# Performance work log

Hardware: AMD Instinct MI355X
Metric: run time of the kernel (lower is better)

## Reference

```python
import jax, jax.numpy as jnp
import numpy as np

# Hard-coded constants from the original module
GAMMA = 0.1      # self.gamma default
N_STEPS = 10     # self.n_steps default
RHO = 0.9        # RMSProp decay
LR = 0.009       # RMSProp learning rate
MOM = 0.9        # momentum
EPS = 1e-8       # RMSProp epsilon
ABS_EPS = 1e-6   # diff_abs smoothing: diff_abs(x) = sqrt(x^2 + 1e-6)

B, IN_DIM, OUT_DIM = 4096, 2048, 4096


def setup_inputs() -> dict:
    key = jax.random.key(0)
    k1, k2 = jax.random.split(key)
    inputs = jax.random.normal(k1, (B, IN_DIM), dtype=jnp.float32)
    # keras 'uniform' init: U(-0.05, 0.05), shape (output_dim, input_dim)
    W = jax.random.uniform(k2, (OUT_DIM, IN_DIM), minval=-0.05, maxval=0.05, dtype=jnp.float32)
    return {"inputs": inputs, "W": W}


def reference(inputs, W):
    batch = inputs.shape[0]
    out_dim = W.shape[0]
    a = jnp.sqrt(inputs * inputs + ABS_EPS)          # diff_abs(inputs), [B, in_dim]
    act = lambda u: 0.5 * (1.0 + jnp.exp(-u))        # self.activation

    def cost(x):
        # l1_norm.sum() + l1_inov + own_norm  (prior = 0)
        l1 = (GAMMA * act(x @ W) * a).sum()
        l1_inov = (GAMMA / 10.0) * jnp.sum(x * x)
        own = GAMMA * jnp.sum(jnp.sqrt(x * x + ABS_EPS))
        return l1 + l1_inov + own

    grad_cost = jax.grad(cost)

    def step(carry, _):
        x, acc1, acc2 = carry
        g = grad_cost(x)                              # [B, out_dim]
        new_acc1 = RHO * acc1 + (1.0 - RHO) * g * g
        denom = jnp.sqrt(new_acc1 + EPS)
        new_acc2 = MOM * acc2 - LR * g / denom
        cand = x - LR * g / denom
        t = 0.1 * LR / denom                          # elementwise prox threshold
        new_x = jnp.maximum(cand - t, 0.0) + jnp.minimum(cand + t, 0.0) + MOM * new_acc2
        new_x = jax.lax.stop_gradient(new_x)          # theano disconnected_grad
        return (new_x, new_acc1, new_acc2), None

    z = jnp.zeros((batch, out_dim), dtype=inputs.dtype)
    # scan runs n_steps; last step's l1_norm uses the state after n_steps-1 updates,
    # so run n_steps-1 updates then compute the final l1_norm directly.
    (x, _, _), _ = jax.lax.scan(step, (z, z, z), None, length=N_STEPS - 1)
    return GAMMA * act(x @ W) * a                     # outputs[-1][-1]: last l1_norm, [B, in_dim]
```

## Files before the change

### kernel.cpp

```cpp
#include <hip/hip_runtime.h>
#include <cstdint>
#include <cstddef>

#define B_DIM   4096
#define IN_DIM  2048
#define OUT_DIM 4096

typedef __attribute__((ext_vector_type(8))) __bf16 bf16x8;
typedef __attribute__((ext_vector_type(4))) float  f32x4;
typedef unsigned short ushortT;

__device__ __forceinline__ ushortT f2bf(float f) {
    unsigned int u = __float_as_uint(f);
    u += 0x7FFFu + ((u >> 16) & 1u);
    return (ushortT)(u >> 16);
}
__device__ __forceinline__ float bf2f(ushortT b) {
    return __uint_as_float(((unsigned int)b) << 16);
}

__device__ __forceinline__ void gload16(const void* g, void* l) {
    __builtin_amdgcn_global_load_lds(
        (const __attribute__((address_space(1))) void*)g,
        (__attribute__((address_space(3))) void*)l, 16, 0, 0);
}

__global__ void prep_g0_kernel(const float* __restrict__ in, ushortT* __restrict__ Gb) {
    int i = blockIdx.x * 256 + threadIdx.x;
    float4 v = reinterpret_cast<const float4*>(in)[i];
    ushort4 g;
    g.x = f2bf(-0.05f * sqrtf(v.x * v.x + 1e-6f));
    g.y = f2bf(-0.05f * sqrtf(v.y * v.y + 1e-6f));
    g.z = f2bf(-0.05f * sqrtf(v.z * v.z + 1e-6f));
    g.w = f2bf(-0.05f * sqrtf(v.w * v.w + 1e-6f));
    reinterpret_cast<ushort4*>(Gb)[i] = g;
}

__global__ void conv_w_kernel(const float* __restrict__ W, ushortT* __restrict__ Wb,
                              ushortT* __restrict__ WTb) {
    __shared__ float tile[64][65];
    const int i0 = blockIdx.x * 64;
    const int j0 = blockIdx.y * 64;
    const int c  = threadIdx.x & 63;
    const int rq = threadIdx.x >> 6;
#pragma unroll
    for (int rp = 0; rp < 16; ++rp) {
        int row = rp * 4 + rq;
        float w = W[(size_t)(j0 + row) * IN_DIM + i0 + c];
        tile[row][c] = w;
        Wb[(size_t)(j0 + row) * IN_DIM + i0 + c] = f2bf(w);
    }
    __syncthreads();
#pragma unroll
    for (int rp = 0; rp < 16; ++rp) {
        int row = rp * 4 + rq;
        WTb[(size_t)(i0 + row) * OUT_DIM + j0 + c] = f2bf(tile[c][row]);
    }
}

#define PHASE(MB, RB, SLOTP, STTILE, C0, NC)                                   \
    {                                                                          \
        const char* sb_ = (SLOTP);                                             \
        if (RB) {                                                              \
            _Pragma("unroll")                                                  \
            for (int n = 0; n < 4; ++n)                                        \
                bF[n] = *reinterpret_cast<const bf16x8*>(sb_ + bRd[n]);        \
        }                                                                      \
        bf16x8 aF[4];                                                          \
        _Pragma("unroll")                                                      \
        for (int m = 0; m < 4; ++m)                                            \
            aF[m] = *reinterpret_cast<const bf16x8*>(sb_ + aRd[(MB) + m]);     \
        if ((STTILE) < nt) {                                                   \
            _Pragma("unroll")                                                  \
            for (int c = 0; c < (NC); ++c) stage_chunk((STTILE), (C0) + c);    \
        }                                                                      \
        __builtin_amdgcn_sched_barrier(0);                                     \
        __builtin_amdgcn_s_barrier();                                          \
        asm volatile("s_waitcnt lgkmcnt(0)" ::: "memory");                     \
        __builtin_amdgcn_sched_barrier(0);                                     \
        __builtin_amdgcn_s_setprio(1);                                         \
        _Pragma("unroll")                                                      \
        for (int m = 0; m < 4; ++m) {                                          \
            _Pragma("unroll")                                                  \
            for (int n = 0; n < 4; ++n)                                        \
                acc[(MB) + m][n] = __builtin_amdgcn_mfma_f32_16x16x32_bf16(    \
                    aF[m], bF[n], acc[(MB) + m][n], 0, 0, 0);                  \
        }                                                                      \
        __builtin_amdgcn_s_setprio(0);                                         \
        __builtin_amdgcn_s_barrier();                                          \
        __builtin_amdgcn_sched_barrier(0);                                     \
    }

template <int EPI, int BM>
__global__ __launch_bounds__(512, 1)
void gemm_phase(const ushortT* __restrict__ A, const ushortT* __restrict__ Bm,
                int N, int K,
                const float* __restrict__ inb, ushortT* __restrict__ Gb,
                float* __restrict__ out,
                ushortT* __restrict__ acc1, ushortT* __restrict__ acc2,
                ushortT* __restrict__ xb) {
    constexpr int BN   = 256;
    constexpr int ASZ  = BM * 64;
    constexpr int BSZ  = BN * 64;
    constexpr int SLOT = ASZ + BSZ;
    constexpr int LA   = BM / 128;
    constexpr int LB   = BN / 128;
    constexpr int L    = LA + LB;
    constexpr int MR   = BM / 32;
    __shared__ alignas(16) char smem[4 * SLOT];

    const int tid  = threadIdx.x;
    const int lane = tid & 63;
    const int w    = tid >> 6;
    const int wm   = w >> 2;
    const int wn   = w & 3;
    const int nbx  = N / BN;
    const int nwg  = gridDim.x;
    const int cpx  = nwg >> 3;
    const int bid  = (int)blockIdx.x;
    const int swz  = (bid & 7) * cpx + (bid >> 3);
    const int bx   = swz % nbx;
    const int by   = swz / nbx;
    const int row0 = by * BM;
    const int col0 = bx * BN;

    const size_t strideK2 = (size_t)K * 2;

    const char* gp[L]; int lo[L];
#pragma unroll
    for (int i = 0; i < LA; ++i) {
        int Lp  = i * 512 + tid;
        int row = Lp >> 2, sl = Lp & 3;
        int src = sl ^ ((row >> 1) & 3);
        gp[i] = (const char*)A + (size_t)(row0 + row) * strideK2 + src * 16;
        lo[i] = i * 8192 + w * 1024;
    }
#pragma unroll
    for (int i = 0; i < LB; ++i) {
        int Lp  = i * 512 + tid;
        int row = Lp >> 2, sl = Lp & 3;
        int src = sl ^ ((row >> 1) & 3);
        gp[LA + i] = (const char*)Bm + (size_t)(col0 + row) * strideK2 + src * 16;
        lo[LA + i] = ASZ + i * 8192 + w * 1024;
    }
    auto stage_all = [&](int tt) {
        char* sb = smem + (tt & 3) * SLOT;
        const size_t kb = (size_t)tt * 64;
#pragma unroll
        for (int c = 0; c < L; ++c) gload16(gp[c] + kb, sb + lo[c]);
    };
    auto stage_chunk = [&](int tt, int c) {
        gload16(gp[c] + (size_t)tt * 64, smem + (tt & 3) * SLOT + lo[c]);
    };

    int aRd[MR], bRd[4];
#pragma unroll
    for (int m = 0; m < MR; ++m) {
        int row = wm * (BM / 2) + m * 16 + (lane & 15);
        aRd[m] = row * 64 + (((lane >> 4) ^ ((row >> 1) & 3)) * 16);
    }
#pragma unroll
    for (int n = 0; n < 4; ++n) {
        int row = wn * 64 + n * 16 + (lane & 15);
        bRd[n] = ASZ + row * 64 + (((lane >> 4) ^ ((row >> 1) & 3)) * 16);
    }

    f32x4 acc[MR][4] = {};
    const int nt = K >> 5;

    stage_all(0); stage_all(1); stage_all(2);

    for (int tt = 0; tt < nt; tt += 2) {
        if (tt + 2 < nt) asm volatile("s_waitcnt vmcnt(%0)" :: "n"(L) : "memory");
        else             asm volatile("s_waitcnt vmcnt(0)"  ::: "memory");
        __builtin_amdgcn_s_barrier();
        __builtin_amdgcn_sched_barrier(0);

        const char* sb0 = smem + (tt & 3) * SLOT;
        const char* sb1 = smem + ((tt + 1) & 3) * SLOT;
        bf16x8 bF[4];
        if constexpr (MR == 8) {
            PHASE(0, true,  sb0, tt + 3, 0, 2)
            PHASE(4, false, sb0, tt + 3, 2, 2)
            PHASE(0, true,  sb1, tt + 4, 0, 2)
            PHASE(4, false, sb1, tt + 4, 2, 2)
        } else {
            PHASE(0, true,  sb0, tt + 3, 0, 3)
            PHASE(0, true,  sb1, tt + 4, 0, 3)
        }
    }

    __builtin_amdgcn_s_barrier();

    float* lep = (float*)(smem + w * 4352);
    const int li = lane >> 4;
    const int lc = lane & 15;
    const int row0w = row0 + wm * (BM / 2);
    const int col0w = col0 + wn * 64;
#pragma unroll
    for (int m = 0; m < MR; ++m) {
#pragma unroll
        for (int n = 0; n < 4; ++n)
#pragma unroll
            for (int i = 0; i < 4; ++i)
                lep[(li * 4 + i) * 68 + n * 16 + lc] = acc[m][n][i];
        asm volatile("s_waitcnt lgkmcnt(0)" ::: "memory");
        __builtin_amdgcn_sched_barrier(0);
#pragma unroll
        for (int rr = 0; rr < 4; ++rr) {
            const int row = rr + li * 4;
            float4 v = *reinterpret_cast<const float4*>(&lep[row * 68 + lc * 4]);
            const size_t idx  = (size_t)(row0w + m * 16 + row) * N + col0w + lc * 4;
            const size_t idx4 = idx >> 2;
            if constexpr (EPI == 0) {
                float4 iv = reinterpret_cast<const float4*>(inb)[idx4];
                ushort4 g;
                g.x = f2bf(-0.05f * sqrtf(iv.x * iv.x + 1e-6f) * expf(-v.x));
                g.y = f2bf(-0.05f * sqrtf(iv.y * iv.y + 1e-6f) * expf(-v.y));
                g.z = f2bf(-0.05f * sqrtf(iv.z * iv.z + 1e-6f) * expf(-v.z));
                g.w = f2bf(-0.05f * sqrtf(iv.w * iv.w + 1e-6f) * expf(-v.w));
                *reinterpret_cast<ushort4*>(&Gb[idx]) = g;
            } else if constexpr (EPI == 1) {
                float4 iv = reinterpret_cast<const float4*>(inb)[idx4];
                float4 o;
                o.x = 0.05f * (1.0f + expf(-v.x)) * sqrtf(iv.x * iv.x + 1e-6f);
                o.y = 0.05f * (1.0f + expf(-v.y)) * sqrtf(iv.y * iv.y + 1e-6f);
                o.z = 0.05f * (1.0f + expf(-v.z)) * sqrtf(iv.z * iv.z + 1e-6f);
                o.w = 0.05f * (1.0f + expf(-v.w)) * sqrtf(iv.w * iv.w + 1e-6f);
                reinterpret_cast<float4*>(out)[idx4] = o;
            } else {
                ushort4 xu  = *reinterpret_cast<const ushort4*>(&xb[idx]);
                ushort4 a1u = *reinterpret_cast<const ushort4*>(&acc1[idx]);
                ushort4 a2u = *reinterpret_cast<const ushort4*>(&acc2[idx]);
                float xs[4] = {bf2f(xu.x), bf2f(xu.y), bf2f(xu.z), bf2f(xu.w)};
                float vs[4] = {v.x, v.y, v.z, v.w};
                ushortT a1s[4] = {a1u.x, a1u.y, a1u.z, a1u.w};
                ushortT a2s[4] = {a2u.x, a2u.y, a2u.z, a2u.w};
                ushortT a1n[4], a2n[4], xbn[4];
#pragma unroll
                for (int j = 0; j < 4; ++j) {
                    float g    = vs[j] + 0.02f * xs[j] + 0.1f * xs[j] * rsqrtf(xs[j] * xs[j] + 1e-6f);
                    float a1   = 0.9f * bf2f(a1s[j]) + 0.1f * g * g;
                    float inv  = rsqrtf(a1 + 1e-8f);
                    float r_   = 0.009f * g * inv;
                    float a2   = 0.9f * bf2f(a2s[j]) - r_;
                    float cand = xs[j] - r_;
                    float t_   = 0.0009f * inv;
                    float xn   = fmaxf(cand - t_, 0.0f) + fminf(cand + t_, 0.0f) + 0.9f * a2;
                    a1n[j] = f2bf(a1); a2n[j] = f2bf(a2); xbn[j] = f2bf(xn);
                }
                *reinterpret_cast<ushort4*>(&acc1[idx]) = make_ushort4(a1n[0], a1n[1], a1n[2], a1n[3]);
                *reinterpret_cast<ushort4*>(&acc2[idx]) = make_ushort4(a2n[0], a2n[1], a2n[2], a2n[3]);
                *reinterpret_cast<ushort4*>(&xb[idx])   = make_ushort4(xbn[0], xbn[1], xbn[2], xbn[3]);
            }
        }
        asm volatile("s_waitcnt lgkmcnt(0)" ::: "memory");
    }
}

extern "C" void kernel_launch(void* const* d_in, const int* in_sizes, int n_in,
                              void* d_out, int out_size, void* d_ws, size_t ws_size,
                              hipStream_t stream) {
    const float* in = (const float*)d_in[0];
    const float* W  = (const float*)d_in[1];
    float* out = (float*)d_out;
    char* ws = (char*)d_ws;

    ushortT* acc1 = (ushortT*)(ws);
    ushortT* acc2 = (ushortT*)(ws + ((size_t)32  << 20));
    ushortT* xb   = (ushortT*)(ws + ((size_t)64  << 20));
    ushortT* Wb   = (ushortT*)(ws + ((size_t)96  << 20));
    ushortT* WTb  = (ushortT*)(ws + ((size_t)112 << 20));
    ushortT* Gb   = (ushortT*)(ws + ((size_t)128 << 20));

    hipMemsetAsync(ws, 0, (size_t)96 << 20, stream);

    prep_g0_kernel<<<dim3(B_DIM * IN_DIM / 4 / 256), dim3(256), 0, stream>>>(in, Gb);
    conv_w_kernel<<<dim3(IN_DIM / 64, OUT_DIM / 64), dim3(256), 0, stream>>>(W, Wb, WTb);

    for (int step = 0; step < 9; ++step) {
        if (step > 0) {
            gemm_phase<0, 128><<<dim3(256), dim3(512), 0, stream>>>(
                xb, WTb, IN_DIM, OUT_DIM, in, Gb, nullptr, nullptr, nullptr, nullptr);
        }
        gemm_phase<2, 256><<<dim3(256), dim3(512), 0, stream>>>(
            Gb, Wb, OUT_DIM, IN_DIM, nullptr, nullptr, nullptr, acc1, acc2, xb);
    }
    gemm_phase<1, 128><<<dim3(256), dim3(512), 0, stream>>>(
        xb, WTb, IN_DIM, OUT_DIM, in, nullptr, out, nullptr, nullptr, nullptr);
}
```

Before: 1.533 ms.

## Add multi-block 256x128 GEMM kernel for the G·W update phase

Replaces the 256x256-tile, 4-stage pipelined kernel used for the RMSProp update GEMM with a new kernel. The new kernel uses 256x128 tiles, double buffering, a smaller LDS footprint and launch bounds that allow several blocks per CU, and it launches 512 workgroups instead of 256. The aim is to raise occupancy and CU utilisation for this GEMM. In exchange it uses a simpler two-stage pipeline with a full vmcnt(0) wait every k-step, which may expose global-load latency. The shared epilogue is moved into a macro.

```diff
diff --git a/kernel.cpp b/kernel.cpp
--- a/kernel.cpp
+++ b/kernel.cpp
@@ -57,6 +57,70 @@
         WTb[(size_t)(i0 + row) * OUT_DIM + j0 + c] = f2bf(tile[c][row]);
     }
 }
+
+#define EPILOGUE(MR_)                                                          \
+    float* lep = (float*)(smem + w * 4352);                                    \
+    const int li = lane >> 4;                                                  \
+    const int lc = lane & 15;                                                  \
+    _Pragma("unroll")                                                          \
+    for (int m = 0; m < (MR_); ++m) {                                          \
+        _Pragma("unroll")                                                      \
+        for (int n = 0; n < 4; ++n)                                            \
+            _Pragma("unroll")                                                  \
+            for (int i = 0; i < 4; ++i)                                        \
+                lep[(li * 4 + i) * 68 + n * 16 + lc] = acc[m][n][i];           \
+        asm volatile("s_waitcnt lgkmcnt(0)" ::: "memory");                     \
+        __builtin_amdgcn_sched_barrier(0);                                     \
+        _Pragma("unroll")                                                      \
+        for (int rr = 0; rr < 4; ++rr) {                                       \
+            const int row = rr + li * 4;                                       \
+            float4 v = *reinterpret_cast<const float4*>(&lep[row * 68 + lc * 4]); \
+            const size_t idx  = (size_t)(row0w + m * 16 + row) * N + col0w + lc * 4; \
+            const size_t idx4 = idx >> 2;                                      \
+            if constexpr (EPI == 0) {                                          \
+                float4 iv = reinterpret_cast<const float4*>(inb)[idx4];        \
+                ushort4 g;                                                     \
+                g.x = f2bf(-0.05f * sqrtf(iv.x * iv.x + 1e-6f) * expf(-v.x));  \
+                g.y = f2bf(-0.05f * sqrtf(iv.y * iv.y + 1e-6f) * expf(-v.y));  \
+                g.z = f2bf(-0.05f * sqrtf(iv.z * iv.z + 1e-6f) * expf(-v.z));  \
+                g.w = f2bf(-0.05f * sqrtf(iv.w * iv.w + 1e-6f) * expf(-v.w));  \
+                *reinterpret_cast<ushort4*>(&Gb[idx]) = g;                     \
+            } else if constexpr (EPI == 1) {                                   \
+                float4 iv = reinterpret_cast<const float4*>(inb)[idx4];        \
+                float4 o;                                                      \
+                o.x = 0.05f * (1.0f + expf(-v.x)) * sqrtf(iv.x * iv.x + 1e-6f); \
+                o.y = 0.05f * (1.0f + expf(-v.y)) * sqrtf(iv.y * iv.y + 1e-6f); \
+                o.z = 0.05f * (1.0f + expf(-v.z)) * sqrtf(iv.z * iv.z + 1e-6f); \
+                o.w = 0.05f * (1.0f + expf(-v.w)) * sqrtf(iv.w * iv.w + 1e-6f); \
+                reinterpret_cast<float4*>(out)[idx4] = o;                      \
+            } else {                                                           \
+                ushort4 xu  = *reinterpret_cast<const ushort4*>(&xb[idx]);     \
+                ushort4 a1u = *reinterpret_cast<const ushort4*>(&acc1[idx]);   \
+                ushort4 a2u = *reinterpret_cast<const ushort4*>(&acc2[idx]);   \
+                float xs[4] = {bf2f(xu.x), bf2f(xu.y), bf2f(xu.z), bf2f(xu.w)}; \
+                float vs[4] = {v.x, v.y, v.z, v.w};                            \
+                ushortT a1s[4] = {a1u.x, a1u.y, a1u.z, a1u.w};                 \
+                ushortT a2s[4] = {a2u.x, a2u.y, a2u.z, a2u.w};                 \
+                ushortT a1n[4], a2n[4], xbn[4];                                \
+                _Pragma("unroll")                                              \
+                for (int j = 0; j < 4; ++j) {                                  \
+                    float g    = vs[j] + 0.02f * xs[j] + 0.1f * xs[j] * rsqrtf(xs[j] * xs[j] + 1e-6f); \
+                    float a1   = 0.9f * bf2f(a1s[j]) + 0.1f * g * g;           \
+                    float inv  = rsqrtf(a1 + 1e-8f);                           \
+                    float r_   = 0.009f * g * inv;                             \
+                    float a2   = 0.9f * bf2f(a2s[j]) - r_;                     \
+                    float cand = xs[j] - r_;                                   \
+                    float t_   = 0.0009f * inv;                                \
+                    float xn   = fmaxf(cand - t_, 0.0f) + fminf(cand + t_, 0.0f) + 0.9f * a2; \
+                    a1n[j] = f2bf(a1); a2n[j] = f2bf(a2); xbn[j] = f2bf(xn);   \
+                }                                                              \
+                *reinterpret_cast<ushort4*>(&acc1[idx]) = make_ushort4(a1n[0], a1n[1], a1n[2], a1n[3]); \
+                *reinterpret_cast<ushort4*>(&acc2[idx]) = make_ushort4(a2n[0], a2n[1], a2n[2], a2n[3]); \
+                *reinterpret_cast<ushort4*>(&xb[idx])   = make_ushort4(xbn[0], xbn[1], xbn[2], xbn[3]); \
+            }                                                                  \
+        }                                                                      \
+        asm volatile("s_waitcnt lgkmcnt(0)" ::: "memory");                     \
+    }
 
 #define PHASE(MB, RB, SLOTP, STTILE, C0, NC)                                   \
     {                                                                          \
@@ -69,7 +133,7 @@
         bf16x8 aF[4];                                                          \
         _Pragma("unroll")                                                      \
         for (int m = 0; m < 4; ++m)                                            \
-            aF[m] = *reinterpret_cast<const bf16x8*>(sb_ + aRd[(MB) + m]);     \
+            aF[m] = *reinterpret_cast<const bf16x8*>(sb_ + aRd[m]);            \
         if ((STTILE) < nt) {                                                   \
             _Pragma("unroll")                                                  \
             for (int c = 0; c < (NC); ++c) stage_chunk((STTILE), (C0) + c);    \
@@ -83,15 +147,15 @@
         for (int m = 0; m < 4; ++m) {                                          \
             _Pragma("unroll")                                                  \
             for (int n = 0; n < 4; ++n)                                        \
-                acc[(MB) + m][n] = __builtin_amdgcn_mfma_f32_16x16x32_bf16(    \
-                    aF[m], bF[n], acc[(MB) + m][n], 0, 0, 0);                  \
+                acc[m][n] = __builtin_amdgcn_mfma_f32_16x16x32_bf16(           \
+                    aF[m], bF[n], acc[m][n], 0, 0, 0);                         \
         }                                                                      \
         __builtin_amdgcn_s_setprio(0);                                         \
         __builtin_amdgcn_s_barrier();                                          \
         __builtin_amdgcn_sched_barrier(0);                                     \
     }
 
-template <int EPI, int BM>
+template <int EPI>
 __global__ __launch_bounds__(512, 1)
 void gemm_phase(const ushortT* __restrict__ A, const ushortT* __restrict__ Bm,
                 int N, int K,
@@ -99,14 +163,10 @@
                 float* __restrict__ out,
                 ushortT* __restrict__ acc1, ushortT* __restrict__ acc2,
                 ushortT* __restrict__ xb) {
-    constexpr int BN   = 256;
+    constexpr int BM = 128, BN = 256;
     constexpr int ASZ  = BM * 64;
-    constexpr int BSZ  = BN * 64;
-    constexpr int SLOT = ASZ + BSZ;
-    constexpr int LA   = BM / 128;
-    constexpr int LB   = BN / 128;
-    constexpr int L    = LA + LB;
-    constexpr int MR   = BM / 32;
+    constexpr int SLOT = ASZ + BN * 64;
+    constexpr int LA   = 1, LB = 2, L = 3;
     __shared__ alignas(16) char smem[4 * SLOT];
 
     const int tid  = threadIdx.x;
@@ -123,7 +183,6 @@
     const int by   = swz / nbx;
     const int row0 = by * BM;
     const int col0 = bx * BN;
-
     const size_t strideK2 = (size_t)K * 2;
 
     const char* gp[L]; int lo[L];
@@ -153,10 +212,10 @@
         gload16(gp[c] + (size_t)tt * 64, smem + (tt & 3) * SLOT + lo[c]);
     };
 
-    int aRd[MR], bRd[4];
-#pragma unroll
-    for (int m = 0; m < MR; ++m) {
-        int row = wm * (BM / 2) + m * 16 + (lane & 15);
+    int aRd[4], bRd[4];
+#pragma unroll
+    for (int m = 0; m < 4; ++m) {
+        int row = wm * 64 + m * 16 + (lane & 15);
         aRd[m] = row * 64 + (((lane >> 4) ^ ((row >> 1) & 3)) * 16);
     }
 #pragma unroll
@@ -165,7 +224,7 @@
         bRd[n] = ASZ + row * 64 + (((lane >> 4) ^ ((row >> 1) & 3)) * 16);
     }
 
-    f32x4 acc[MR][4] = {};
+    f32x4 acc[4][4] = {};
     const int nt = K >> 5;
 
     stage_all(0); stage_all(1); stage_all(2);
@@ -179,83 +238,112 @@
         const char* sb0 = smem + (tt & 3) * SLOT;
         const char* sb1 = smem + ((tt + 1) & 3) * SLOT;
         bf16x8 bF[4];
-        if constexpr (MR == 8) {
-            PHASE(0, true,  sb0, tt + 3, 0, 2)
-            PHASE(4, false, sb0, tt + 3, 2, 2)
-            PHASE(0, true,  sb1, tt + 4, 0, 2)
-            PHASE(4, false, sb1, tt + 4, 2, 2)
-        } else {
-            PHASE(0, true,  sb0, tt + 3, 0, 3)
-            PHASE(0, true,  sb1, tt + 4, 0, 3)
-        }
+        PHASE(0, true, sb0, tt + 3, 0, 3)
+        PHASE(0, true, sb1, tt + 4, 0, 3)
     }
 
     __builtin_amdgcn_s_barrier();
-
-    float* lep = (float*)(smem + w * 4352);
-    const int li = lane >> 4;
-    const int lc = lane & 15;
-    const int row0w = row0 + wm * (BM / 2);
+    const int row0w = row0 + wm * 64;
     const int col0w = col0 + wn * 64;
-#pragma unroll
-    for (int m = 0; m < MR; ++m) {
-#pragma unroll
-        for (int n = 0; n < 4; ++n)
-#pragma unroll
-            for (int i = 0; i < 4; ++i)
-                lep[(li * 4 + i) * 68 + n * 16 + lc] = acc[m][n][i];
-        asm volatile("s_waitcnt lgkmcnt(0)" ::: "memory");
+    EPILOGUE(4)
+}
+
+template <int EPI>
+__global__ __launch_bounds__(512, 4)
+void gemm_mb2(const ushortT* __restrict__ A, const ushortT* __restrict__ Bm,
+              int N, int K,
+              const float* __restrict__ inb, ushortT* __restrict__ Gb,
+              float* __restrict__ out,
+              ushortT* __restrict__ acc1, ushortT* __restrict__ acc2,
+              ushortT* __restrict__ xb) {
+    constexpr int BM = 256, BN = 128;
+    constexpr int ASZ  = BM * 64;
+    constexpr int SLOT = ASZ + BN * 64;
+    constexpr int CA   = 2, CB = 1, L = 3;
+    __shared__ alignas(16) char smem[2 * SLOT];
+
+    const int tid  = threadIdx.x;
+    const int lane = tid & 63;
+    const int w    = tid >> 6;
+    const int wm   = w >> 1;
+    const int wn   = w & 1;
+    const int nbx  = N / BN;
+    const int nwg  = gridDim.x;
+    const int cpx  = nwg >> 3;
+    const int bid  = (int)blockIdx.x;
+    const int swz  = (bid & 7) * cpx + (bid >> 3);
+    const int bx   = swz % nbx;
+    const int by   = swz / nbx;
+    const int row0 = by * BM;
+    const int col0 = bx * BN;
+    const size_t strideK2 = (size_t)K * 2;
+
+    const char* gp[L]; int lo[L];
+#pragma unroll
+    for (int c = 0; c < CA; ++c) {
+        int Lp  = c * 512 + tid;
+        int row = Lp >> 2, sl = Lp & 3;
+        int src = sl ^ ((row >> 1) & 3);
+        gp[c] = (const char*)A + (size_t)(row0 + row) * strideK2 + src * 16;
+        lo[c] = c * 8192 + w * 1024;
+    }
+#pragma unroll
+    for (int c = 0; c < CB; ++c) {
+        int Lp  = c * 512 + tid;
+        int row = Lp >> 2, sl = Lp & 3;
+        int src = sl ^ ((row >> 1) & 3);
+        gp[CA + c] = (const char*)Bm + (size_t)(col0 + row) * strideK2 + src * 16;
+        lo[CA + c] = ASZ + c * 8192 + w * 1024;
+    }
+    auto stage = [&](int tt) {
+        char* sb = smem + (tt & 1) * SLOT;
+        const size_t kb = (size_t)tt * 64;
+#pragma unroll
+        for (int c = 0; c < L; ++c) gload16(gp[c] + kb, sb + lo[c]);
+    };
+
+    int aRd[4], bRd[4];
+#pragma unroll
+    for (int m = 0; m < 4; ++m) {
+        int row = wm * 64 + m * 16 + (lane & 15);
+        aRd[m] = row * 64 + (((lane >> 4) ^ ((row >> 1) & 3)) * 16);
+    }
+#pragma unroll
+    for (int n = 0; n < 4; ++n) {
+        int row = wn * 64 + n * 16 + (lane & 15);
+        bRd[n] = ASZ + row * 64 + (((lane >> 4) ^ ((row >> 1) & 3)) * 16);
+    }
+
+    f32x4 acc[4][4] = {};
+    const int nt = K >> 5;
+
+    stage(0);
+
+    for (int tt = 0; tt < nt; ++tt) {
+        asm volatile("s_waitcnt vmcnt(0)" ::: "memory");
+        __builtin_amdgcn_s_barrier();
         __builtin_amdgcn_sched_barrier(0);
-#pragma unroll
-        for (int rr = 0; rr < 4; ++rr) {
-            const int row = rr + li * 4;
-            float4 v = *reinterpret_cast<const float4*>(&lep[row * 68 + lc * 4]);
-            const size_t idx  = (size_t)(row0w + m * 16 + row) * N + col0w + lc * 4;
-            const size_t idx4 = idx >> 2;
-            if constexpr (EPI == 0) {
-                float4 iv = reinterpret_cast<const float4*>(inb)[idx4];
-                ushort4 g;
-                g.x = f2bf(-0.05f * sqrtf(iv.x * iv.x + 1e-6f) * expf(-v.x));
-                g.y = f2bf(-0.05f * sqrtf(iv.y * iv.y + 1e-6f) * expf(-v.y));
-                g.z = f2bf(-0.05f * sqrtf(iv.z * iv.z + 1e-6f) * expf(-v.z));
-                g.w = f2bf(-0.05f * sqrtf(iv.w * iv.w + 1e-6f) * expf(-v.w));
-                *reinterpret_cast<ushort4*>(&Gb[idx]) = g;
-            } else if constexpr (EPI == 1) {
-                float4 iv = reinterpret_cast<const float4*>(inb)[idx4];
-                float4 o;
-                o.x = 0.05f * (1.0f + expf(-v.x)) * sqrtf(iv.x * iv.x + 1e-6f);
-                o.y = 0.05f * (1.0f + expf(-v.y)) * sqrtf(iv.y * iv.y + 1e-6f);
-                o.z = 0.05f * (1.0f + expf(-v.z)) * sqrtf(iv.z * iv.z + 1e-6f);
-                o.w = 0.05f * (1.0f + expf(-v.w)) * sqrtf(iv.w * iv.w + 1e-6f);
-                reinterpret_cast<float4*>(out)[idx4] = o;
-            } else {
-                ushort4 xu  = *reinterpret_cast<const ushort4*>(&xb[idx]);
-                ushort4 a1u = *reinterpret_cast<const ushort4*>(&acc1[idx]);
-                ushort4 a2u = *reinterpret_cast<const ushort4*>(&acc2[idx]);
-                float xs[4] = {bf2f(xu.x), bf2f(xu.y), bf2f(xu.z), bf2f(xu.w)};
-                float vs[4] = {v.x, v.y, v.z, v.w};
-                ushortT a1s[4] = {a1u.x, a1u.y, a1u.z, a1u.w};
-                ushortT a2s[4] = {a2u.x, a2u.y, a2u.z, a2u.w};
-                ushortT a1n[4], a2n[4], xbn[4];
-#pragma unroll
-                for (int j = 0; j < 4; ++j) {
-                    float g    = vs[j] + 0.02f * xs[j] + 0.1f * xs[j] * rsqrtf(xs[j] * xs[j] + 1e-6f);
-                    float a1   = 0.9f * bf2f(a1s[j]) + 0.1f * g * g;
-                    float inv  = rsqrtf(a1 + 1e-8f);
-                    float r_   = 0.009f * g * inv;
-                    float a2   = 0.9f * bf2f(a2s[j]) - r_;
-                    float cand = xs[j] - r_;
-                    float t_   = 0.0009f * inv;
-                    float xn   = fmaxf(cand - t_, 0.0f) + fminf(cand + t_, 0.0f) + 0.9f * a2;
-                    a1n[j] = f2bf(a1); a2n[j] = f2bf(a2); xbn[j] = f2bf(xn);
-                }
-                *reinterpret_cast<ushort4*>(&acc1[idx]) = make_ushort4(a1n[0], a1n[1], a1n[2], a1n[3]);
-                *reinterpret_cast<ushort4*>(&acc2[idx]) = make_ushort4(a2n[0], a2n[1], a2n[2], a2n[3]);
-                *reinterpret_cast<ushort4*>(&xb[idx])   = make_ushort4(xbn[0], xbn[1], xbn[2], xbn[3]);
-            }
-        }
-        asm volatile("s_waitcnt lgkmcnt(0)" ::: "memory");
-    }
+
+        const char* sb = smem + (tt & 1) * SLOT;
+        bf16x8 aF[4], bF[4];
+#pragma unroll
+        for (int n = 0; n < 4; ++n) bF[n] = *reinterpret_cast<const bf16x8*>(sb + bRd[n]);
+#pragma unroll
+        for (int m = 0; m < 4; ++m) aF[m] = *reinterpret_cast<const bf16x8*>(sb + aRd[m]);
+        if (tt + 1 < nt) stage(tt + 1);
+        __builtin_amdgcn_s_setprio(1);
+#pragma unroll
+        for (int m = 0; m < 4; ++m)
+#pragma unroll
+            for (int n = 0; n < 4; ++n)
+                acc[m][n] = __builtin_amdgcn_mfma_f32_16x16x32_bf16(aF[m], bF[n], acc[m][n], 0, 0, 0);
+        __builtin_amdgcn_s_setprio(0);
+    }
+
+    __builtin_amdgcn_s_barrier();
+    const int row0w = row0 + wm * 64;
+    const int col0w = col0 + wn * 64;
+    EPILOGUE(4)
 }
 
 extern "C" void kernel_launch(void* const* d_in, const int* in_sizes, int n_in,
@@ -280,12 +368,12 @@
 
     for (int step = 0; step < 9; ++step) {
         if (step > 0) {
-            gemm_phase<0, 128><<<dim3(256), dim3(512), 0, stream>>>(
+            gemm_phase<0><<<dim3(256), dim3(512), 0, stream>>>(
                 xb, WTb, IN_DIM, OUT_DIM, in, Gb, nullptr, nullptr, nullptr, nullptr);
         }
-        gemm_phase<2, 256><<<dim3(256), dim3(512), 0, stream>>>(
+        gemm_mb2<2><<<dim3(512), dim3(512), 0, stream>>>(
             Gb, Wb, OUT_DIM, IN_DIM, nullptr, nullptr, nullptr, acc1, acc2, xb);
     }
-    gemm_phase<1, 128><<<dim3(256), dim3(512), 0, stream>>>(
+    gemm_phase<1><<<dim3(256), dim3(512), 0, stream>>>(
         xb, WTb, IN_DIM, OUT_DIM, in, nullptr, out, nullptr, nullptr, nullptr);
 }
```

Result: slower. 1.576 ms (+2.8%).
